# Kernel tuning notes

Hardware: AMD Instinct MI355X
Metric: run time of the kernel (lower is better)

## Reference

```python
import jax, jax.numpy as jnp
import numpy as np

H = 768        # spanbert_out
WF = 20        # width_encoding_feature_size
MSW = 10       # max_span_width
TOP_RATIO = 0.4
MAX_ANTE = 50
DEPTH = 2      # coref_depth
D = 3 * H + WF # span_rep_size = 2324
NEG = -1e30


def setup_inputs() -> dict:
    key = jax.random.key(0)
    ks = jax.random.split(key, 12)
    W, G = 2048, 100
    seq = jax.random.normal(ks[0], (W, H), jnp.float32)
    sentence_map = jnp.sort(jax.random.randint(ks[1], (W,), 0, 64))
    gold_starts = jax.random.randint(ks[2], (G,), 0, W)
    gold_ends = jnp.clip(gold_starts + jax.random.randint(ks[3], (G,), 0, MSW), 0, W - 1)
    cluster_ids = jax.random.randint(ks[4], (G,), 0, 20)
    s = 0.02
    return {
        "sequence_output": seq,
        "W_alpha": jax.random.normal(ks[5], (H, 1), jnp.float32) * s,
        "b_alpha": jnp.zeros((1,), jnp.float32),
        "W_m": jax.random.normal(ks[6], (D, 1), jnp.float32) * s,
        "b_m": jnp.zeros((1,), jnp.float32),
        "W_c": jax.random.normal(ks[7], (D, D), jnp.float32) * s,
        "W_a": jax.random.normal(ks[8], (3 * D, 1), jnp.float32) * s,
        "b_a": jnp.zeros((1,), jnp.float32),
        "W_f": jax.random.normal(ks[9], (2 * D, D), jnp.float32) * s,
        "b_f": jnp.zeros((D,), jnp.float32),
        "width_feats": jax.random.normal(ks[10], (MSW, WF), jnp.float32) * s,
        "sentence_map": sentence_map,
        "gold_starts": gold_starts,
        "gold_ends": gold_ends,
        "cluster_ids": cluster_ids,
    }


def _forward(seq, W_alpha, b_alpha, W_m, b_m, W_c, W_a, b_a, W_f, b_f, width_feats,
             sentence_map, gold_starts, gold_ends, cluster_ids):
    W = seq.shape[0]
    # candidate spans: [W, MSW] -> flat [N], N = W*MSW
    cs = jnp.broadcast_to(jnp.arange(W)[:, None], (W, MSW)).reshape(-1)
    ce = (jnp.arange(W)[:, None] + jnp.arange(MSW)[None, :]).reshape(-1)
    ce_c = jnp.minimum(ce, W - 1)
    valid = (ce < W) & (sentence_map[cs] == sentence_map[ce_c])  # [N]

    # candidate cluster labels (get_candidate_labels): sum cluster ids of exact gold matches
    same_span = (cs[:, None] == gold_starts[None, :]) & (ce_c[:, None] == gold_ends[None, :])
    cand_cluster = jnp.sum(jnp.where(same_span, cluster_ids[None, :], 0), axis=1)  # [N]

    # span representations
    start_emb = seq[cs]                               # [N,H]
    end_emb = seq[ce_c]                               # [N,H]
    alphas = (seq @ W_alpha + b_alpha)[:, 0]          # [W]
    doc_range = jnp.arange(W)[None, :]
    mmask = (doc_range >= cs[:, None]) & (doc_range <= ce_c[:, None])  # [N,W]
    attn = jax.nn.softmax(jnp.where(mmask, alphas[None, :], NEG), axis=1)
    span_emb = attn @ seq                             # [N,H]
    widths = jnp.clip(ce_c - cs, 0, MSW - 1)          # width - 1
    rep = jnp.concatenate([start_emb, end_emb, span_emb, width_feats[widths]], axis=1)  # [N,D]

    # mention scoring + top-m pruning (masked_select replaced by -inf masking)
    mention_scores = (rep @ W_m + b_m)[:, 0]          # [N]
    masked_scores = jnp.where(valid, mention_scores, NEG)
    m = int(TOP_RATIO * W)
    _, top_idx = jax.lax.top_k(masked_scores, m)
    top_idx = jnp.sort(top_idx)
    top_rep = rep[top_idx]                            # [m,D]
    ts, te = cs[top_idx], ce_c[top_idx]
    tscore = mention_scores[top_idx]
    tcluster = cand_cluster[top_idx]

    # prune antecedents
    k = min(m, MAX_ANTE)
    offsets = jnp.arange(m)[:, None] - jnp.arange(m)[None, :]
    amask = offsets >= 1
    fast = tscore[:, None] + tscore[None, :] + jnp.where(amask, 0.0, NEG)
    fast = fast + (top_rep @ W_c) @ top_rep.T         # [m,m]
    _, top_ante = jax.lax.top_k(fast, k)              # [m,k]
    ta_mask = jnp.take_along_axis(amask, top_ante, axis=1)
    ta_fast = jnp.take_along_axis(fast, top_ante, axis=1)

    # iterative attention-weighted antecedent aggregation with gated update
    dummy = jnp.zeros((m, 1), seq.dtype)
    reps = top_rep
    scores_a = ta_fast
    for _ in range(DEPTH):
        ante_emb = reps[top_ante]                     # [m,k,D]
        tgt = reps[:, None, :]
        pair = jnp.concatenate(
            [jnp.broadcast_to(tgt, (m, k, D)), ante_emb, ante_emb * tgt], axis=2)  # [m,k,3D]
        slow = (pair @ W_a)[:, :, 0] + b_a[0]         # [m,k]
        scores_a = ta_fast + slow
        wts = jax.nn.softmax(jnp.concatenate([dummy, scores_a], axis=1), axis=1)  # [m,k+1]
        full = jnp.concatenate([reps[:, None, :], ante_emb], axis=1)              # [m,k+1,D]
        attended = jnp.sum(wts[:, :, None] * full, axis=1)                        # [m,D]
        f = jax.nn.sigmoid(jnp.concatenate([reps, attended], axis=1) @ W_f + b_f)
        reps = f * attended + (1.0 - f) * reps

    final_scores = jnp.concatenate([dummy, scores_a], axis=1)  # [m,k+1]

    # antecedent labels and marginal log-likelihood loss
    ante_cluster = jnp.where(ta_mask, tcluster[top_ante], -1)
    pairwise = (ante_cluster == tcluster[:, None]) & (tcluster > 0)[:, None]
    dummy_lab = ~jnp.any(pairwise, axis=1, keepdims=True)
    lab = jnp.concatenate([dummy_lab, pairwise], axis=1)
    gold_scores = jnp.where(lab, final_scores, NEG)
    loss = jnp.sum(jax.nn.logsumexp(final_scores, axis=1) - jax.nn.logsumexp(gold_scores, axis=1))
    return ts, te, top_ante, final_scores, loss


def reference(sequence_output, W_alpha, b_alpha, W_m, b_m, W_c, W_a, b_a, W_f, b_f,
              width_feats, sentence_map, gold_starts, gold_ends, cluster_ids):
    return _forward(sequence_output, W_alpha, b_alpha, W_m, b_m, W_c, W_a, b_a,
                    W_f, b_f, width_feats, sentence_map, gold_starts, gold_ends, cluster_ids)
```

## Files before the change

### kernel.cpp

```cpp
#include <hip/hip_runtime.h>
#include <cfloat>
#include <climits>
#include <math.h>

#define HD   768
#define MSW  10
#define WFK  20
#define DD   2324
#define K2   50
#define NEGF (-1e30f)

#define KPAD 2432
#define KAW  4864
#define MPAD 896
#define NPAD 2432

typedef __attribute__((ext_vector_type(8))) short    s8b;
typedef __attribute__((ext_vector_type(8))) unsigned short u16x8;
typedef __attribute__((ext_vector_type(4))) float    f32x4;

__device__ inline unsigned short f2bf(float f){
  unsigned u = __float_as_uint(f);
  unsigned r = (u + 0x7FFFu + ((u >> 16) & 1u)) >> 16;
  return (unsigned short)r;
}
__device__ inline float bf2f(unsigned short h){
  return __uint_as_float(((unsigned)h) << 16);
}

__device__ __forceinline__ void gload16(const unsigned short* g, void* l){
  __builtin_amdgcn_global_load_lds(
      (const __attribute__((address_space(1))) void*)g,
      (__attribute__((address_space(3))) void*)l, 16, 0, 0);
}

__device__ __forceinline__ int swz_col(int row, int col){
  return col ^ ((row & 7) << 3);
}

__device__ __forceinline__ void xcd_remap(int &bx, int &by, int &bz){
  int nwg  = (int)(gridDim.x*gridDim.y*gridDim.z);
  int orig = (int)(blockIdx.x + gridDim.x*(blockIdx.y + gridDim.y*blockIdx.z));
  int q = nwg >> 3, r = nwg & 7;
  int x8 = orig & 7, o8 = orig >> 3;
  int wg = (x8 < r ? x8*(q+1) : r*(q+1) + (x8-r)*q) + o8;
  bx = wg % (int)gridDim.x;
  int tmp = wg / (int)gridDim.x;
  by = tmp % (int)gridDim.y;
  bz = tmp / (int)gridDim.y;
}

__global__ void row_proj(const float* __restrict__ seq, const float* __restrict__ Wa,
                         const float* __restrict__ ba, const float* __restrict__ Wm,
                         float* alphas, float* p1, float* p2, float* p3, int W){
  int w = blockIdx.x; int tid = threadIdx.x;
  const float* row = seq + (size_t)w * HD;
  float s0=0.f, s1=0.f, s2=0.f, s3=0.f;
  for(int h=tid; h<HD; h+=256){
    float x = row[h];
    s0 += x * Wa[h];
    s1 += x * Wm[h];
    s2 += x * Wm[HD + h];
    s3 += x * Wm[2*HD + h];
  }
  __shared__ float r0[256], r1[256], r2[256], r3[256];
  r0[tid]=s0; r1[tid]=s1; r2[tid]=s2; r3[tid]=s3;
  __syncthreads();
  for(int st=128; st>0; st>>=1){
    if(tid<st){ r0[tid]+=r0[tid+st]; r1[tid]+=r1[tid+st]; r2[tid]+=r2[tid+st]; r3[tid]+=r3[tid+st]; }
    __syncthreads();
  }
  if(tid==0){ alphas[w]=r0[0]+ba[0]; p1[w]=r1[0]; p2[w]=r2[0]; p3[w]=r3[0]; }
}

__global__ void mention_kernel(const float* __restrict__ alphas, const float* __restrict__ p1,
                               const float* __restrict__ p2, const float* __restrict__ p3,
                               const float* __restrict__ wfeat, const float* __restrict__ Wm,
                               const float* __restrict__ bm,
                               const int* __restrict__ smap, const int* __restrict__ gs,
                               const int* __restrict__ ge, const int* __restrict__ cid, int G,
                               float* mscore, float* mmask, int* ccl, int W){
  int c = blockIdx.x*blockDim.x + threadIdx.x;
  int C = W * MSW;
  if(c >= C) return;
  int s = c / MSW, r = c - s*MSW;
  int e = s + r; int ec = min(e, W-1);
  int L = ec - s;
  bool valid = (e < W) && (smap[s] == smap[ec]);
  float maxa = -FLT_MAX;
  for(int j=0;j<=L;j++) maxa = fmaxf(maxa, alphas[s+j]);
  float sum=0.f, sdot=0.f;
  for(int j=0;j<=L;j++){ float ee = expf(alphas[s+j]-maxa); sum += ee; sdot += ee*p3[s+j]; }
  sdot /= sum;
  float wp=0.f;
  for(int f=0; f<WFK; f++) wp += wfeat[L*WFK+f] * Wm[3*HD+f];
  float ms = p1[s] + p2[ec] + sdot + wp + bm[0];
  mscore[c] = ms;
  mmask[c]  = valid ? ms : NEGF;
  int cc = 0;
  for(int g=0; g<G; g++) if(s==gs[g] && ec==ge[g]) cc += cid[g];
  ccl[c] = cc;
}

__device__ inline unsigned fkey(float f){
  unsigned b = __float_as_uint(f);
  return (b & 0x80000000u) ? ~b : (b | 0x80000000u);
}

__global__ __launch_bounds__(1024)
void select_kernel(const float* __restrict__ mmask, const float* __restrict__ mscore,
                   const int* __restrict__ ccl, int m, int C, int W,
                   int* top_idx, float* tscore, int* tclust,
                   float* out_ts, float* out_te){
  const int T = 1024;
  int tid = threadIdx.x;
  int chunk = (C + T - 1)/T;
  int lo = tid*chunk, hi = min(lo+chunk, C);
  int n = hi - lo; if(n < 0) n = 0;
  unsigned kb[32];
  for(int t=0;t<n;t++) kb[t] = fkey(mmask[lo+t]);

  __shared__ unsigned s_hist[256];
  __shared__ unsigned s_scan[1024];
  __shared__ unsigned s_pref;
  __shared__ int s_rem;
  if(tid==0){ s_pref=0u; s_rem=m; }
  __syncthreads();

  for(int b=3;b>=0;b--){
    if(tid<256) s_hist[tid]=0u;
    __syncthreads();
    unsigned pref = s_pref;
    unsigned msk = (b==3)?0u:(0xFFFFFFFFu << ((b+1)*8));
    for(int t=0;t<n;t++){
      unsigned u = kb[t];
      if((u & msk)==pref) atomicAdd(&s_hist[(u>>(b*8))&0xFFu], 1u);
    }
    __syncthreads();
    if(tid==0){
      int rem = s_rem; unsigned acc=0u; int bin;
      for(bin=255;bin>=1;bin--){
        unsigned h = s_hist[bin];
        if(acc + h >= (unsigned)rem) break;
        acc += h;
      }
      if(bin < 0) bin = 0;
      s_pref = pref | ((unsigned)bin << (b*8));
      s_rem = rem - (int)acc;
    }
    __syncthreads();
  }
  unsigned Tk = s_pref;
  int need = s_rem;

  unsigned nG=0, nE=0;
  for(int t=0;t<n;t++){ unsigned u=kb[t]; nG += (u>Tk)?1u:0u; nE += (u==Tk)?1u:0u; }

  s_scan[tid]=nE; __syncthreads();
  for(int off=1; off<T; off<<=1){
    unsigned x = (tid>=off)? s_scan[tid-off]:0u; __syncthreads();
    s_scan[tid]+=x; __syncthreads();
  }
  unsigned eqBase = s_scan[tid]-nE;
  __syncthreads();

  int takeLeft = need - (int)eqBase;
  int take = takeLeft<0?0:(takeLeft>(int)nE?(int)nE:takeLeft);
  unsigned selCnt = nG + (unsigned)take;

  s_scan[tid]=selCnt; __syncthreads();
  for(int off=1; off<T; off<<=1){
    unsigned x = (tid>=off)? s_scan[tid-off]:0u; __syncthreads();
    s_scan[tid]+=x; __syncthreads();
  }
  unsigned posBase = s_scan[tid]-selCnt;

  int pos = (int)posBase; int eq = (int)eqBase;
  for(int t=0;t<n;t++){
    unsigned u = kb[t];
    bool sel = false;
    if(u>Tk) sel=true;
    else if(u==Tk){ if(eq<need) sel=true; eq++; }
    if(sel){
      int c = lo+t;
      top_idx[pos] = c;
      int s = c/MSW, r = c - s*MSW; int e = min(s + r, W-1);
      tscore[pos] = mscore[c];
      tclust[pos] = ccl[c];
      out_ts[pos] = (float)s;
      out_te[pos] = (float)e;
      pos++;
    }
  }
}

__global__ void build_rep(const float* __restrict__ seq, const float* __restrict__ alphas,
                          const float* __restrict__ wfeat, const int* __restrict__ top_idx,
                          float* rep, int W){
  int i = blockIdx.x; int tid = threadIdx.x;
  int c = top_idx[i];
  int s = c/MSW, r = c - s*MSW; int ec = min(s + r, W-1); int L = ec - s;
  float wv[MSW];
  float maxa = -FLT_MAX;
  for(int j=0;j<=L;j++) maxa = fmaxf(maxa, alphas[s+j]);
  float sum = 0.f;
  for(int j=0;j<=L;j++){ wv[j] = expf(alphas[s+j]-maxa); sum += wv[j]; }
  float inv = 1.f/sum;
  float* o = rep + (size_t)i*DD;
  for(int d=tid; d<HD; d+=256){
    o[d]      = seq[(size_t)s*HD + d];
    o[HD+d]   = seq[(size_t)ec*HD + d];
    float sp = 0.f;
    for(int j=0;j<=L;j++) sp += wv[j]*seq[(size_t)(s+j)*HD + d];
    o[2*HD+d] = sp*inv;
  }
  for(int f=tid; f<WFK; f+=256) o[3*HD+f] = wfeat[L*WFK+f];
}

__global__ void conv_split(const float* __restrict__ src, int rows, int cols,
                           unsigned short* __restrict__ hi, unsigned short* __restrict__ lo,
                           float* __restrict__ ztgt, int zn){
  int idx = blockIdx.x*256 + threadIdx.x;
  if(idx >= MPAD*KPAD) return;
  if(idx < zn) ztgt[idx] = 0.f;
  int row = idx / KPAD, col = idx - row*KPAD;
  float v = (row < rows && col < cols) ? src[(size_t)row*cols + col] : 0.f;
  unsigned short h = f2bf(v);
  int w = row*KPAD + swz_col(row, col);
  hi[w] = h;
  lo[w] = f2bf(v - bf2f(h));
}

__global__ void conv_split_wcT(const float* __restrict__ Wc,
                               unsigned short* __restrict__ WtH, unsigned short* __restrict__ WtL){
  int n  = blockIdx.y*64 + threadIdx.x;
  int k8 = blockIdx.x*8;
  u16x8 vh, vl;
  #pragma unroll
  for(int j=0;j<8;j++){
    int k = k8 + j;
    float f = (n < DD && k < DD) ? Wc[(size_t)k*DD + n] : 0.f;
    unsigned short h = f2bf(f);
    vh[j] = h;
    vl[j] = f2bf(f - bf2f(h));
  }
  int k8s = swz_col(n, k8);
  *(u16x8*)(WtH + (size_t)n*KPAD + k8s) = vh;
  *(u16x8*)(WtL + (size_t)n*KPAD + k8s) = vl;
}

__global__ void conv_slow_ops(const float* __restrict__ cur, const float* __restrict__ Wa3,
                              unsigned short* __restrict__ CurBf, unsigned short* __restrict__ Xbf,
                              float* __restrict__ bilin, int mm, int m){
  int idx = blockIdx.x*256 + threadIdx.x;
  if(idx >= MPAD*KPAD) return;
  if(idx < mm) bilin[idx] = 0.f;
  int row = idx / KPAD, col = idx - row*KPAD;
  float v = 0.f, w = 0.f;
  if(row < m && col < DD){ v = cur[(size_t)row*DD + col]; w = Wa3[2*DD + col]; }
  int ws = row*KPAD + swz_col(row, col);
  CurBf[ws] = f2bf(v);
  Xbf[ws]   = f2bf(v * w);
}

__global__ __launch_bounds__(256,2)
void gemm_split3_sk(const unsigned short* __restrict__ Ah, const unsigned short* __restrict__ Al,
                    const unsigned short* __restrict__ Bth, const unsigned short* __restrict__ Btl,
                    float* __restrict__ C, int M, int N, int ldc){
  __shared__ __align__(16) unsigned short sAh[128*64];
  __shared__ __align__(16) unsigned short sAl[128*64];
  __shared__ __align__(16) unsigned short sBh[128*64];
  __shared__ __align__(16) unsigned short sBl[128*64];
  int bx, by, bz; xcd_remap(bx, by, bz);
  int t = threadIdx.x;
  int row0 = by*128, col0 = bx*128;
  const int tiles = KPAD/64;
  int per = (tiles + (int)gridDim.z - 1)/(int)gridDim.z;
  int tb = min(bz*per, tiles), te = min(tb + per, tiles);
  if(tb >= te) return;
  int lane = t&63, w = t>>6;
  int wr = (w>>1)*64, wc = (w&1)*64;
  int quad = lane>>4, l15 = lane&15;
  int seg = lane&7;
  size_t ro = (size_t)(w*8 + (lane>>3));
  const unsigned short* gAh = Ah  + ((size_t)row0 + ro)*KPAD + seg*8;
  const unsigned short* gAl = Al  + ((size_t)row0 + ro)*KPAD + seg*8;
  const unsigned short* gBh = Bth + ((size_t)col0 + ro)*KPAD + seg*8;
  const unsigned short* gBl = Btl + ((size_t)col0 + ro)*KPAD + seg*8;
  const int lds0 = (w*8)*64;
  const int c0 = ((quad ^ (l15 & 7)) << 3);

  f32x4 acc[4][4];
  #pragma unroll
  for(int mi=0;mi<4;mi++)
    #pragma unroll
    for(int ni=0;ni<4;ni++) acc[mi][ni] = (f32x4){0.f,0.f,0.f,0.f};

  for(int kt=tb; kt<te; ++kt){
    size_t k0 = (size_t)kt*64;
    #pragma unroll
    for(int r=0;r<4;r++){
      size_t go = (size_t)(r*32)*KPAD + k0;
      int lo = lds0 + r*32*64;
      gload16(gAh + go, sAh + lo);
      gload16(gAl + go, sAl + lo);
      gload16(gBh + go, sBh + lo);
      gload16(gBl + go, sBl + lo);
    }
    __syncthreads();
    #pragma unroll
    for(int ks=0;ks<2;ks++){
      const int co = c0 ^ (ks<<5);
      s8b fah[4], fal[4], fbh[4], fbl[4];
      #pragma unroll
      for(int mi=0;mi<4;mi++){
        int ra = (wr+mi*16+l15)*64 + co;
        fah[mi] = *(const s8b*)&sAh[ra];
        fal[mi] = *(const s8b*)&sAl[ra];
      }
      #pragma unroll
      for(int ni=0;ni<4;ni++){
        int rb = (wc+ni*16+l15)*64 + co;
        fbh[ni] = *(const s8b*)&sBh[rb];
        fbl[ni] = *(const s8b*)&sBl[rb];
      }
      #pragma unroll
      for(int mi=0;mi<4;mi++)
        #pragma unroll
        for(int ni=0;ni<4;ni++){
          acc[mi][ni] = __builtin_amdgcn_mfma_f32_16x16x32_bf16(fah[mi], fbh[ni], acc[mi][ni], 0,0,0);
          acc[mi][ni] = __builtin_amdgcn_mfma_f32_16x16x32_bf16(fah[mi], fbl[ni], acc[mi][ni], 0,0,0);
          acc[mi][ni] = __builtin_amdgcn_mfma_f32_16x16x32_bf16(fal[mi], fbh[ni], acc[mi][ni], 0,0,0);
        }
    }
    __syncthreads();
  }

  #pragma unroll
  for(int ni=0;ni<4;ni++){
    int gn = col0 + wc + ni*16 + l15;
    if(gn >= N) continue;
    #pragma unroll
    for(int mi=0;mi<4;mi++){
      #pragma unroll
      for(int rg=0;rg<4;rg++){
        int gr = row0 + wr + mi*16 + quad*4 + rg;
        if(gr >= M) continue;
        atomicAdd(&C[(size_t)gr*ldc + gn], acc[mi][ni][rg]);
      }
    }
  }
}

__global__ __launch_bounds__(256,2)
void gemm_bf16_m97(const unsigned short* __restrict__ A, const unsigned short* __restrict__ Bt,
                   float* __restrict__ C, int M, int N, int ldc, int ldk, int tiles){
  __shared__ __align__(16) unsigned short sA[2][128*64];
  __shared__ __align__(16) unsigned short sB[2][128*64];
  int bx, by, bz; xcd_remap(bx, by, bz);
  int t = threadIdx.x;
  int row0 = by*128, col0 = bx*128;
  int per = (tiles + (int)gridDim.z - 1)/(int)gridDim.z;
  int tb = min(bz*per, tiles), te = min(tb + per, tiles);
  if(tb >= te) return;
  int lane = t&63, w = t>>6;
  int wr = (w>>1)*64, wc = (w&1)*64;
  int quad = lane>>4, l15 = lane&15;
  int seg = lane&7;
  size_t ro = (size_t)(w*8 + (lane>>3));
  const unsigned short* gA = A  + ((size_t)row0 + ro)*ldk + seg*8;
  const unsigned short* gB = Bt + ((size_t)col0 + ro)*ldk + seg*8;
  const int lds0 = (w*8)*64;
  const int c0 = ((quad ^ (l15 & 7)) << 3);

  f32x4 acc[4][4];
  #pragma unroll
  for(int mi=0;mi<4;mi++)
    #pragma unroll
    for(int ni=0;ni<4;ni++) acc[mi][ni] = (f32x4){0.f,0.f,0.f,0.f};

  auto STAGE = [&](int b, int kt){
    size_t k0 = (size_t)kt*64;
    #pragma unroll
    for(int r=0;r<4;r++){
      size_t go = (size_t)(r*32)*ldk + k0;
      int lo = lds0 + r*32*64;
      gload16(gA + go, &sA[b][lo]);
      gload16(gB + go, &sB[b][lo]);
    }
  };

  STAGE(0, tb);
  __syncthreads();
  int buf = 0;
  for(int kt=tb; kt<te; ++kt){
    if(kt+1 < te) STAGE(buf^1, kt+1);
    #pragma unroll
    for(int ks=0;ks<2;ks++){
      const int co = c0 ^ (ks<<5);
      s8b fa[4], fb[4];
      #pragma unroll
      for(int mi=0;mi<4;mi++) fa[mi] = *(const s8b*)&sA[buf][(wr+mi*16+l15)*64 + co];
      #pragma unroll
      for(int ni=0;ni<4;ni++) fb[ni] = *(const s8b*)&sB[buf][(wc+ni*16+l15)*64 + co];
      #pragma unroll
      for(int mi=0;mi<4;mi++)
        #pragma unroll
        for(int ni=0;ni<4;ni++)
          acc[mi][ni] = __builtin_amdgcn_mfma_f32_16x16x32_bf16(fa[mi], fb[ni], acc[mi][ni], 0,0,0);
    }
    __syncthreads();
    buf ^= 1;
  }

  #pragma unroll
  for(int ni=0;ni<4;ni++){
    int gn = col0 + wc + ni*16 + l15;
    if(gn >= N) continue;
    #pragma unroll
    for(int mi=0;mi<4;mi++){
      #pragma unroll
      for(int rg=0;rg<4;rg++){
        int gr = row0 + wr + mi*16 + quad*4 + rg;
        if(gr >= M) continue;
        atomicAdd(&C[(size_t)gr*ldc + gn], acc[mi][ni][rg]);
      }
    }
  }
}

#define NT 13
__global__ void topante_kernel(const float* __restrict__ tscore, const float* __restrict__ bilin,
                               int m, int* ante, float* tafast, float* out_ante){
  int i = blockIdx.x; int lane = threadIdx.x;
  float tsi = tscore[i];
  float v[NT];
  #pragma unroll
  for(int t=0;t<NT;t++){
    int j = lane + t*64;
    float f = -FLT_MAX;
    if(j < m){
      f = tsi + tscore[j];
      f += (j < i) ? 0.f : NEGF;
      f += bilin[(size_t)i*m + j];
    }
    v[t] = f;
  }
  unsigned consumed = 0u;
  int r_ante = 0; float r_fast = 0.f;
  for(int it=0; it<K2; ++it){
    float lv = -FLT_MAX; int li = m;
    #pragma unroll
    for(int t=0;t<NT;t++){
      bool live = ((consumed >> t) & 1u) == 0u;
      if(live && v[t] > lv){ lv = v[t]; li = lane + t*64; }
    }
    float bv = lv; int bi = li;
    #pragma unroll
    for(int off=32; off>0; off>>=1){
      float ov = __shfl_xor(bv, off);
      int   oi = __shfl_xor(bi, off);
      if(ov > bv || (ov == bv && oi < bi)){ bv = ov; bi = oi; }
    }
    if(bi < m && (bi & 63) == lane) consumed |= (1u << (bi >> 6));
    if(lane == it){ r_ante = bi; r_fast = bv; }
  }
  if(lane < K2){
    ante[(size_t)i*K2 + lane]   = r_ante;
    tafast[(size_t)i*K2 + lane] = r_fast;
    out_ante[(size_t)i*K2+lane] = (float)r_ante;
  }
}

__global__ void uv_kernel(const float* __restrict__ reps, const float* __restrict__ Wa3,
                          float* u, float* v, int m){
  int i = blockIdx.x; int tid = threadIdx.x;
  const float* rp = reps + (size_t)i*DD;
  float s1=0.f, s2=0.f;
  for(int d=tid; d<DD; d+=256){ float x = rp[d]; s1 += x*Wa3[d]; s2 += x*Wa3[DD+d]; }
  __shared__ float r1[256], r2[256];
  r1[tid]=s1; r2[tid]=s2; __syncthreads();
  for(int st=128; st>0; st>>=1){
    if(tid<st){ r1[tid]+=r1[tid+st]; r2[tid]+=r2[tid+st]; }
    __syncthreads();
  }
  if(tid==0){ u[i]=r1[0]; v[i]=r2[0]; }
}

__global__ void slow_gather(const float* __restrict__ P, const float* __restrict__ u,
                            const float* __restrict__ v, const int* __restrict__ ante,
                            const float* __restrict__ tafast, const float* __restrict__ ba,
                            float* sc, int m){
  int p = blockIdx.x*256 + threadIdx.x;
  if(p >= m*K2) return;
  int i = p / K2; int j = ante[p];
  sc[p] = tafast[p] + u[i] + v[j] + P[(size_t)i*m + j] + ba[0];
}

__global__ void attend_kernel(const float* __restrict__ reps, const float* __restrict__ sc,
                              const int* __restrict__ ante, float* att, int m){
  int i = blockIdx.x; int tid = threadIdx.x;
  __shared__ float wts[K2+1];
  __shared__ float scs[K2];
  __shared__ int   js[K2];
  if(tid < K2){ scs[tid] = sc[(size_t)i*K2 + tid]; js[tid] = ante[(size_t)i*K2 + tid]; }
  __syncthreads();
  if(tid==0){
    float mx = 0.f;
    for(int t=0;t<K2;t++) mx = fmaxf(mx, scs[t]);
    float sum = expf(0.f - mx); wts[0] = sum;
    for(int t=0;t<K2;t++){ float e = expf(scs[t]-mx); wts[t+1]=e; sum += e; }
    float inv = 1.f/sum;
    for(int t=0;t<=K2;t++) wts[t] *= inv;
  }
  __syncthreads();
  const float* ri_ = reps + (size_t)i*DD;
  for(int d=tid; d<DD; d+=256){
    float a = wts[0]*ri_[d];
    for(int t=0;t<K2;t++) a += wts[t+1]*reps[(size_t)js[t]*DD + d];
    att[(size_t)i*DD + d] = a;
  }
}

__global__ void conv_acat(const float* __restrict__ cur, const float* __restrict__ att,
                          unsigned short* __restrict__ A,
                          float* __restrict__ nxt, int total, int m){
  int idx = blockIdx.x*256 + threadIdx.x;
  if(idx >= MPAD*KAW) return;
  if(idx < total) nxt[idx] = 0.f;
  int row = idx / KAW, col = idx - row*KAW;
  float v = 0.f;
  if(row < m){
    if(col < DD) v = cur[(size_t)row*DD + col];
    else if(col >= KPAD && col < KPAD + DD) v = att[(size_t)row*DD + (col - KPAD)];
  }
  A[row*KAW + swz_col(row, col)] = f2bf(v);
}

__global__ void conv_wf(const float* __restrict__ Wf, unsigned short* __restrict__ Bt){
  int n  = blockIdx.y*64 + threadIdx.x;
  int k8 = blockIdx.x*8;
  int s  = (k8 >= KPAD) ? 1 : 0;
  int kk = k8 - s*KPAD;
  u16x8 v;
  #pragma unroll
  for(int j=0;j<8;j++){
    int k = kk + j;
    float f = (n < DD && k < DD) ? Wf[(size_t)(s*DD + k)*DD + n] : 0.f;
    v[j] = f2bf(f);
  }
  int k8s = swz_col(n, k8);
  *(u16x8*)(Bt + (size_t)n*KAW + k8s) = v;
}

__global__ void gate_update(const float* __restrict__ bfv, const float* __restrict__ att,
                            const float* __restrict__ cur, float* __restrict__ nxt, int total){
  int idx = blockIdx.x*256 + threadIdx.x;
  if(idx >= total) return;
  int col = idx % DD;
  float pre = nxt[idx] + bfv[col];
  float g = 1.f/(1.f + expf(-pre));
  nxt[idx] = g*att[idx] + (1.f - g)*cur[idx];
}

__global__ void final_loss(const float* __restrict__ sc, const int* __restrict__ ante,
                           const int* __restrict__ tclust, float* out_fs, float* row_loss, int m){
  int i = blockIdx.x*blockDim.x + threadIdx.x;
  if(i >= m) return;
  int tci = tclust[i];
  unsigned long long labm = 0ull;
  bool anyp = false;
  float mx = 0.f;
  float mg = -FLT_MAX;
  for(int t=0;t<K2;t++){
    float v = sc[(size_t)i*K2 + t];
    mx = fmaxf(mx, v);
    int j = ante[(size_t)i*K2 + t];
    bool mk = (j < i);
    int ac = mk ? tclust[j] : -1;
    bool p = (ac == tci) && (tci > 0);
    if(p){ labm |= (1ull << (t+1)); anyp = true; mg = fmaxf(mg, v); }
  }
  if(!anyp){ labm |= 1ull; mg = 0.f; }
  float s1 = expf(0.f - mx);
  float s2 = (labm & 1ull) ? expf(0.f - mg) : 0.f;
  float* o = out_fs + (size_t)i*(K2+1);
  o[0] = 0.f;
  for(int t=0;t<K2;t++){
    float v = sc[(size_t)i*K2 + t];
    o[t+1] = v;
    s1 += expf(v - mx);
    if(labm & (1ull << (t+1))) s2 += expf(v - mg);
  }
  row_loss[i] = (mx + logf(s1)) - (mg + logf(s2));
}

__global__ void loss_sum(const float* __restrict__ row_loss, float* out, int m){
  int tid = threadIdx.x;
  float s = 0.f;
  for(int i=tid; i<m; i+=256) s += row_loss[i];
  __shared__ float red[256];
  red[tid]=s; __syncthreads();
  for(int st=128; st>0; st>>=1){ if(tid<st) red[tid]+=red[tid+st]; __syncthreads(); }
  if(tid==0) out[0] = red[0];
}

extern "C" void kernel_launch(void* const* d_in, const int* in_sizes, int n_in,
                              void* d_out, int out_size, void* d_ws, size_t ws_size,
                              hipStream_t stream){
  const int W = in_sizes[11];
  const int G = in_sizes[12];
  const int C = W * MSW;
  const int m = (int)(0.4 * (double)W);

  const float* seq   = (const float*)d_in[0];
  const float* Wal   = (const float*)d_in[1];
  const float* bal   = (const float*)d_in[2];
  const float* Wm    = (const float*)d_in[3];
  const float* bm    = (const float*)d_in[4];
  const float* Wc    = (const float*)d_in[5];
  const float* WaA   = (const float*)d_in[6];
  const float* baA   = (const float*)d_in[7];
  const float* Wf    = (const float*)d_in[8];
  const float* bf    = (const float*)d_in[9];
  const float* wfeat = (const float*)d_in[10];
  const int*   smap  = (const int*)d_in[11];
  const int*   gs    = (const int*)d_in[12];
  const int*   ge    = (const int*)d_in[13];
  const int*   cid   = (const int*)d_in[14];
  float* out = (float*)d_out;

  char* ws = (char*)d_ws;
  size_t off = 0;
  auto alloc = [&](size_t bytes)->char*{
    char* p = ws + off;
    off += (bytes + 255) & ~(size_t)255;
    return p;
  };
  const size_t PLANE  = (size_t)MPAD*KPAD*2;
  const size_t WPLANE = (size_t)NPAD*KPAD*2;

  float* alphas  = (float*)alloc((size_t)W*4);
  float* p1      = (float*)alloc((size_t)W*4);
  float* p2      = (float*)alloc((size_t)W*4);
  float* p3      = (float*)alloc((size_t)W*4);
  float* mscore  = (float*)alloc((size_t)C*4);
  float* mmask   = (float*)alloc((size_t)C*4);
  int*   ccl     = (int*)  alloc((size_t)C*4);
  int*   top_idx = (int*)  alloc((size_t)m*4);
  float* tscore  = (float*)alloc((size_t)m*4);
  int*   tclust  = (int*)  alloc((size_t)m*4);
  float* B1      = (float*)alloc((size_t)m*DD*4);
  float* B2      = (float*)alloc((size_t)m*DD*4);
  float* B3      = (float*)alloc((size_t)m*DD*4);
  float* bilin   = (float*)alloc((size_t)m*m*4);
  int*   ante    = (int*)  alloc((size_t)m*K2*4);
  float* tafast  = (float*)alloc((size_t)m*K2*4);
  float* uB      = (float*)alloc((size_t)m*4);
  float* vB      = (float*)alloc((size_t)m*4);
  float* scB     = (float*)alloc((size_t)m*K2*4);
  float* rloss   = (float*)alloc((size_t)m*4);
  char* regionA = alloc(2*PLANE);
  unsigned short* RepH  = (unsigned short*)regionA;
  unsigned short* RepL  = (unsigned short*)(regionA + PLANE);
  unsigned short* XbfA  = (unsigned short*)regionA;
  unsigned short* CurBf = (unsigned short*)(regionA + PLANE);
  unsigned short* Acat  = (unsigned short*)regionA;
  char* regionB = alloc(2*WPLANE);
  unsigned short* WtH  = (unsigned short*)regionB;
  unsigned short* WtL  = (unsigned short*)(regionB + WPLANE);
  unsigned short* A2H  = (unsigned short*)regionB;
  unsigned short* A2L  = (unsigned short*)(regionB + PLANE);
  unsigned short* BtWf = (unsigned short*)regionB;

  float* out_ts   = out;
  float* out_te   = out + m;
  float* out_ante = out + 2*m;
  float* out_fs   = out + 2*m + (size_t)m*K2;
  float* out_loss = out + 2*m + (size_t)m*K2 + (size_t)m*(K2+1);

  row_proj<<<W, 256, 0, stream>>>(seq, Wal, bal, Wm, alphas, p1, p2, p3, W);
  mention_kernel<<<(C+255)/256, 256, 0, stream>>>(alphas, p1, p2, p3, wfeat, Wm, bm,
                                                  smap, gs, ge, cid, G,
                                                  mscore, mmask, ccl, W);
  select_kernel<<<1, 1024, 0, stream>>>(mmask, mscore, ccl, m, C, W,
                                        top_idx, tscore, tclust, out_ts, out_te);
  build_rep<<<m, 256, 0, stream>>>(seq, alphas, wfeat, top_idx, B1, W);
  {
    const int NEL = MPAD*KPAD;
    conv_split<<<(NEL+255)/256, 256, 0, stream>>>(B1, m, DD, RepH, RepL, B2, m*DD);
    dim3 gw(KPAD/8, NPAD/64);
    conv_split_wcT<<<gw, 64, 0, stream>>>(Wc, WtH, WtL);
    dim3 g1(NPAD/128, MPAD/128, 3);
    gemm_split3_sk<<<g1, 256, 0, stream>>>(RepH, RepL, WtH, WtL, B2, m, DD, DD);
    conv_split<<<(NEL+255)/256, 256, 0, stream>>>(B2, m, DD, A2H, A2L, bilin, m*m);
    dim3 g2(MPAD/128, MPAD/128, 10);
    gemm_split3_sk<<<g2, 256, 0, stream>>>(A2H, A2L, RepH, RepL, bilin, m, m, m);
  }
  topante_kernel<<<m, 64, 0, stream>>>(tscore, bilin, m, ante, tafast, out_ante);
  {
    dim3 g(KAW/8, NPAD/64);
    conv_wf<<<g, 64, 0, stream>>>(Wf, BtWf);
  }

  float* cur = B1; float* nxt = B2;
  const int NEL = MPAD*KPAD;
  const int total = m * DD;
  for(int depth=0; depth<2; depth++){
    uv_kernel<<<m, 256, 0, stream>>>(cur, WaA, uB, vB, m);
    conv_slow_ops<<<(NEL+255)/256, 256, 0, stream>>>(cur, WaA, CurBf, XbfA, bilin, m*m, m);
    dim3 gp(MPAD/128, MPAD/128, 10);
    gemm_bf16_m97<<<gp, 256, 0, stream>>>(XbfA, CurBf, bilin, m, m, m, KPAD, KPAD/64);
    slow_gather<<<(m*K2+255)/256, 256, 0, stream>>>(bilin, uB, vB, ante, tafast, baA, scB, m);
    attend_kernel<<<m, 256, 0, stream>>>(cur, scB, ante, B3, m);
    conv_acat<<<(MPAD*KAW+255)/256, 256, 0, stream>>>(cur, B3, Acat, nxt, total, m);
    dim3 gg(NPAD/128, MPAD/128, 3);
    gemm_bf16_m97<<<gg, 256, 0, stream>>>(Acat, BtWf, nxt, m, DD, DD, KAW, KAW/64);
    gate_update<<<(total+255)/256, 256, 0, stream>>>(bf, B3, cur, nxt, total);
    float* t = cur; cur = nxt; nxt = t;
  }

  final_loss<<<(m+255)/256, 256, 0, stream>>>(scB, ante, tclust, out_fs, rloss, m);
  loss_sum<<<1, 256, 0, stream>>>(rloss, out_loss, m);
}
```

Baseline: 797.7 us.

## Compute slow antecedent scores directly for top-K pairs instead of full m×m GEMM

Replaces the per-depth bf16 conversion, the full m×m bilinear GEMM and the gather kernel with a single kernel. For each mention it dots the Wa3-scaled row against only its 50 selected antecedent rows in fp32. This drops most of the work, since only m×50 of the m×m products are ever used, and removes two launches and the conversion traffic per depth. The new path also computes in fp32 rather than bf16, so numerics change slightly.

```diff
diff --git a/kernel.cpp b/kernel.cpp
--- a/kernel.cpp
+++ b/kernel.cpp
@@ -249,20 +249,6 @@
   *(u16x8*)(WtL + (size_t)n*KPAD + k8s) = vl;
 }
 
-__global__ void conv_slow_ops(const float* __restrict__ cur, const float* __restrict__ Wa3,
-                              unsigned short* __restrict__ CurBf, unsigned short* __restrict__ Xbf,
-                              float* __restrict__ bilin, int mm, int m){
-  int idx = blockIdx.x*256 + threadIdx.x;
-  if(idx >= MPAD*KPAD) return;
-  if(idx < mm) bilin[idx] = 0.f;
-  int row = idx / KPAD, col = idx - row*KPAD;
-  float v = 0.f, w = 0.f;
-  if(row < m && col < DD){ v = cur[(size_t)row*DD + col]; w = Wa3[2*DD + col]; }
-  int ws = row*KPAD + swz_col(row, col);
-  CurBf[ws] = f2bf(v);
-  Xbf[ws]   = f2bf(v * w);
-}
-
 __global__ __launch_bounds__(256,2)
 void gemm_split3_sk(const unsigned short* __restrict__ Ah, const unsigned short* __restrict__ Al,
                     const unsigned short* __restrict__ Bth, const unsigned short* __restrict__ Btl,
@@ -487,14 +473,34 @@
   if(tid==0){ u[i]=r1[0]; v[i]=r2[0]; }
 }
 
-__global__ void slow_gather(const float* __restrict__ P, const float* __restrict__ u,
-                            const float* __restrict__ v, const int* __restrict__ ante,
-                            const float* __restrict__ tafast, const float* __restrict__ ba,
-                            float* sc, int m){
-  int p = blockIdx.x*256 + threadIdx.x;
-  if(p >= m*K2) return;
-  int i = p / K2; int j = ante[p];
-  sc[p] = tafast[p] + u[i] + v[j] + P[(size_t)i*m + j] + ba[0];
+__global__ __launch_bounds__(256)
+void slow_scores(const float* __restrict__ cur, const float* __restrict__ Wa3,
+                 const float* __restrict__ u, const float* __restrict__ v,
+                 const int* __restrict__ ante, const float* __restrict__ tafast,
+                 const float* __restrict__ ba, float* __restrict__ sc, int m){
+  int i = blockIdx.x;
+  int tid = threadIdx.x;
+  int lane = tid & 63, w = tid >> 6;
+  __shared__ __align__(16) float xi[DD];
+  const float* ri = cur + (size_t)i*DD;
+  for(int k=tid; k<DD; k+=256) xi[k] = ri[k]*Wa3[2*DD + k];
+  __syncthreads();
+  const float ui = u[i], b0 = ba[0];
+  const int D4 = DD/4;
+  const f32x4* xi4 = (const f32x4*)xi;
+  for(int t=w; t<K2; t+=4){
+    int j = ante[(size_t)i*K2 + t];
+    const f32x4* rj4 = (const f32x4*)(cur + (size_t)j*DD);
+    float s = 0.f;
+    for(int k=lane; k<D4; k+=64){
+      f32x4 a = xi4[k], b = rj4[k];
+      s += a[0]*b[0] + a[1]*b[1] + a[2]*b[2] + a[3]*b[3];
+    }
+    #pragma unroll
+    for(int off=32; off>0; off>>=1) s += __shfl_xor(s, off);
+    if(lane==0)
+      sc[(size_t)i*K2 + t] = tafast[(size_t)i*K2 + t] + ui + v[j] + s + b0;
+  }
 }
 
 __global__ void attend_kernel(const float* __restrict__ reps, const float* __restrict__ sc,
@@ -663,8 +669,6 @@
   char* regionA = alloc(2*PLANE);
   unsigned short* RepH  = (unsigned short*)regionA;
   unsigned short* RepL  = (unsigned short*)(regionA + PLANE);
-  unsigned short* XbfA  = (unsigned short*)regionA;
-  unsigned short* CurBf = (unsigned short*)(regionA + PLANE);
   unsigned short* Acat  = (unsigned short*)regionA;
   char* regionB = alloc(2*WPLANE);
   unsigned short* WtH  = (unsigned short*)regionB;
@@ -704,14 +708,10 @@
   }
 
   float* cur = B1; float* nxt = B2;
-  const int NEL = MPAD*KPAD;
   const int total = m * DD;
   for(int depth=0; depth<2; depth++){
     uv_kernel<<<m, 256, 0, stream>>>(cur, WaA, uB, vB, m);
-    conv_slow_ops<<<(NEL+255)/256, 256, 0, stream>>>(cur, WaA, CurBf, XbfA, bilin, m*m, m);
-    dim3 gp(MPAD/128, MPAD/128, 10);
-    gemm_bf16_m97<<<gp, 256, 0, stream>>>(XbfA, CurBf, bilin, m, m, m, KPAD, KPAD/64);
-    slow_gather<<<(m*K2+255)/256, 256, 0, stream>>>(bilin, uB, vB, ante, tafast, baA, scB, m);
+    slow_scores<<<m, 256, 0, stream>>>(cur, WaA, uB, vB, ante, tafast, baA, scB, m);
     attend_kernel<<<m, 256, 0, stream>>>(cur, scB, ante, B3, m);
     conv_acat<<<(MPAD*KAW+255)/256, 256, 0, stream>>>(cur, B3, Acat, nxt, total, m);
     dim3 gg(NPAD/128, MPAD/128, 3);
```

Result: no change. 793.9 us (-0.5%).
